# Kernel optimization log

Measured on AMD Instinct MI355X. Metric: run time of the kernel, lower is better.

## Reference

```python
import jax, jax.numpy as jnp
import numpy as np

DECAY = 0.99
BETA = 0.25
EPS_NORM = 1e-12  # matches F.normalize eps


def _l2_normalize(x):
    n = jnp.linalg.norm(x, axis=-1, keepdims=True)
    return x / jnp.maximum(n, EPS_NORM)


def setup_inputs() -> dict:
    key = jax.random.key(0)
    ks = jax.random.split(key, 8)
    B, C, H, W = 16, 256, 64, 64
    D, K = 16, 4096  # codebook_dim, n_embed
    z = jax.random.normal(ks[0], (B, C, H, W), dtype=jnp.float32)
    # 1x1 convs == per-pixel linear layers
    w_down = jax.random.normal(ks[1], (D, C), dtype=jnp.float32) / np.sqrt(C).astype(np.float32)
    b_down = jnp.zeros((D,), dtype=jnp.float32)
    w_up = jax.random.normal(ks[2], (C, D), dtype=jnp.float32) / np.sqrt(D).astype(np.float32)
    b_up = jnp.zeros((C,), dtype=jnp.float32)
    embedding = jax.random.uniform(ks[3], (K, D), minval=-1.0 / K, maxval=1.0 / K, dtype=jnp.float32)
    cluster_size = jax.random.uniform(ks[4], (K,), minval=0.5, maxval=2.0, dtype=jnp.float32)
    embed_avg = jax.random.normal(ks[5], (K, D), dtype=jnp.float32) * 0.01
    return {"z": z, "w_down": w_down, "b_down": b_down, "w_up": w_up,
            "b_up": b_up, "embedding": embedding,
            "cluster_size": cluster_size, "embed_avg": embed_avg}


def reference(z, w_down, b_down, w_up, b_up, embedding, cluster_size, embed_avg):
    B, C, H, W = z.shape
    K, D = embedding.shape

    # proj_down: 1x1 conv -> per-token linear
    z_low = jnp.einsum('bchw,dc->bdhw', z, w_down) + b_down[None, :, None, None]
    z_flat = z_low.transpose(0, 2, 3, 1).reshape(-1, D)          # [N, D]
    z_norm = _l2_normalize(z_flat)
    e_norm = _l2_normalize(embedding)                             # [K, D]

    # squared L2 distances (argmin identical to cdist argmin)
    d2 = (jnp.sum(z_norm * z_norm, -1, keepdims=True)
          - 2.0 * z_norm @ e_norm.T
          + jnp.sum(e_norm * e_norm, -1)[None, :])               # [N, K]
    indices = jnp.argmin(d2, axis=-1)                             # [N]
    z_q_flat = e_norm[indices]                                    # [N, D]

    # EMA buffer update (training path); scatter-accumulate via segment_sum
    ones = jnp.ones(indices.shape, dtype=jnp.float32)
    batch_cluster_size = jax.ops.segment_sum(ones, indices, num_segments=K)
    batch_embed_sum = jax.ops.segment_sum(z_norm, indices, num_segments=K)
    new_cluster_size = cluster_size * DECAY + (1.0 - DECAY) * batch_cluster_size
    new_embed_avg = embed_avg * DECAY + (1.0 - DECAY) * batch_embed_sum
    n = new_cluster_size.sum()
    cs = (new_cluster_size + 1e-5) / (n + K * 1e-5) * n
    new_embedding = new_embed_avg / cs[:, None]

    commitment_loss = BETA * jnp.mean((z_norm - jax.lax.stop_gradient(z_q_flat)) ** 2)

    # straight-through estimator
    z_q_low_flat = z_norm + jax.lax.stop_gradient(z_q_flat - z_norm)
    z_q_low = z_q_low_flat.reshape(B, H, W, D).transpose(0, 3, 1, 2)
    z_q = jnp.einsum('bdhw,cd->bchw', z_q_low, w_up) + b_up[None, :, None, None]

    indices_2d = indices.reshape(B, H, W)

    # metrics / entropy loss (usage == bincount(indices))
    usage_prob = batch_cluster_size / (batch_cluster_size.sum() + 1e-8)
    entropy = -jnp.sum(usage_prob * jnp.log(usage_prob + 1e-8))
    entropy_loss = jnp.log(jnp.float32(K)) - entropy

    return (z_q, commitment_loss, indices_2d, entropy_loss,
            new_embedding, new_cluster_size, new_embed_avg)
```

## Files before the change

kernel.cpp:

```cpp
#include <hip/hip_runtime.h>
#include <math.h>

#define NTOK 65536
#define CDIM 256
#define DDIM 16
#define KCOD 4096
#define HWSZ 4096

#define KSPLIT 16
#define CPS (KCOD / KSPLIT)
#define TPT 4
#define TBLK (256 * TPT)

#define WS_ENORM 0
#define WS_ENN   (WS_ENORM + KCOD*DDIM)
#define WS_WDT   (WS_ENN + KCOD)
#define WS_ZN    (WS_WDT + CDIM*DDIM)
#define WS_BCS   (WS_ZN + NTOK*DDIM)
#define WS_BES   (WS_BCS + KCOD)
#define WS_SCAL  (WS_BES + KCOD*DDIM)
#define WS_PACK  (WS_SCAL + 8)

#define OFS_ZQ   0
#define OFS_LOSS 16777216
#define OFS_IDX  16777217
#define OFS_ENT  16842753
#define OFS_NE   16842754
#define OFS_NCS  16908290
#define OFS_NEA  16912386

__global__ __launch_bounds__(256) void knorm_kernel(const float* __restrict__ emb,
                                                    const float* __restrict__ w_down,
                                                    float* __restrict__ ws) {
  int k = blockIdx.x * 256 + threadIdx.x;
  const float4* src = (const float4*)emb + (size_t)k * 4;
  float4 t0 = src[0], t1 = src[1], t2 = src[2], t3 = src[3];
  float e[16] = {t0.x,t0.y,t0.z,t0.w, t1.x,t1.y,t1.z,t1.w,
                 t2.x,t2.y,t2.z,t2.w, t3.x,t3.y,t3.z,t3.w};
  float ss = 0.f;
  #pragma unroll
  for (int d = 0; d < 16; ++d) ss += e[d] * e[d];
  float dn = fmaxf(sqrtf(ss), 1e-12f);
  #pragma unroll
  for (int d = 0; d < 16; ++d) e[d] = e[d] / dn;
  float s2 = 0.f;
  #pragma unroll
  for (int d = 0; d < 16; ++d) s2 += e[d] * e[d];
  float4* dst = (float4*)(ws + WS_ENORM) + (size_t)k * 4;
  dst[0] = make_float4(e[0],e[1],e[2],e[3]);
  dst[1] = make_float4(e[4],e[5],e[6],e[7]);
  dst[2] = make_float4(e[8],e[9],e[10],e[11]);
  dst[3] = make_float4(e[12],e[13],e[14],e[15]);
  ws[WS_ENN + k] = s2;
  ws[WS_WDT + k] = w_down[(k & 15) * 256 + (k >> 4)];
}

__global__ __launch_bounds__(256) void kdown_kernel(const float* __restrict__ z,
                                                    const float* __restrict__ wdt,
                                                    const float* __restrict__ b_down,
                                                    float* __restrict__ znp) {
  const int tid = threadIdx.x;
  const int n = blockIdx.x * 256 + tid;
  const int b = n >> 12;
  const int hw = n & 4095;

  const float* zp = z + (size_t)b * (CDIM * HWSZ) + hw;
  float acc[16];
  #pragma unroll
  for (int d = 0; d < 16; ++d) acc[d] = 0.f;
  #pragma unroll 8
  for (int c = 0; c < CDIM; ++c) {
    float zv = zp[(size_t)c * HWSZ];
    const float4* wr = (const float4*)(wdt + c * 16);
    float4 w0 = wr[0], w1 = wr[1], w2 = wr[2], w3 = wr[3];
    acc[0]  = fmaf(zv, w0.x, acc[0]);  acc[1]  = fmaf(zv, w0.y, acc[1]);
    acc[2]  = fmaf(zv, w0.z, acc[2]);  acc[3]  = fmaf(zv, w0.w, acc[3]);
    acc[4]  = fmaf(zv, w1.x, acc[4]);  acc[5]  = fmaf(zv, w1.y, acc[5]);
    acc[6]  = fmaf(zv, w1.z, acc[6]);  acc[7]  = fmaf(zv, w1.w, acc[7]);
    acc[8]  = fmaf(zv, w2.x, acc[8]);  acc[9]  = fmaf(zv, w2.y, acc[9]);
    acc[10] = fmaf(zv, w2.z, acc[10]); acc[11] = fmaf(zv, w2.w, acc[11]);
    acc[12] = fmaf(zv, w3.x, acc[12]); acc[13] = fmaf(zv, w3.y, acc[13]);
    acc[14] = fmaf(zv, w3.z, acc[14]); acc[15] = fmaf(zv, w3.w, acc[15]);
  }
  #pragma unroll
  for (int d = 0; d < 16; ++d) acc[d] = acc[d] + b_down[d];
  float ss = 0.f;
  #pragma unroll
  for (int d = 0; d < 16; ++d) ss += acc[d] * acc[d];
  float dn = fmaxf(sqrtf(ss), 1e-12f);
  float zn[16];
  #pragma unroll
  for (int d = 0; d < 16; ++d) zn[d] = acc[d] / dn;

  float4* op = (float4*)znp + (size_t)n * 4;
  op[0] = make_float4(zn[0],zn[1],zn[2],zn[3]);
  op[1] = make_float4(zn[4],zn[5],zn[6],zn[7]);
  op[2] = make_float4(zn[8],zn[9],zn[10],zn[11]);
  op[3] = make_float4(zn[12],zn[13],zn[14],zn[15]);
}

__global__ __launch_bounds__(256, 4) void kscan_kernel(const float* __restrict__ enorm,
                                                       const float* __restrict__ ennp,
                                                       const float* __restrict__ znp,
                                                       unsigned long long* __restrict__ packp) {
  __shared__ float ecache[CPS * DDIM];
  __shared__ float encache[CPS];

  const int tid = threadIdx.x;
  const int kbase = blockIdx.y * CPS;

  {
    const float4* s4 = (const float4*)(enorm + (size_t)kbase * 16);
    float4* d4 = (float4*)ecache;
    #pragma unroll
    for (int i = 0; i < 4; ++i) d4[tid + i * 256] = s4[tid + i * 256];
    encache[tid] = ennp[kbase + tid];
  }
  __syncthreads();

  float nz[TPT][16];
  float best[TPT];
  int bidx[TPT];
  const int tokbase = blockIdx.x * TBLK + tid;
  {
    const float4* zp = (const float4*)znp;
    #pragma unroll
    for (int p = 0; p < TPT; ++p) {
      int tok = tokbase + p * 256;
      float4 a0 = zp[(size_t)tok * 4 + 0];
      float4 a1 = zp[(size_t)tok * 4 + 1];
      float4 a2 = zp[(size_t)tok * 4 + 2];
      float4 a3 = zp[(size_t)tok * 4 + 3];
      nz[p][0]=-2.f*a0.x; nz[p][1]=-2.f*a0.y; nz[p][2]=-2.f*a0.z; nz[p][3]=-2.f*a0.w;
      nz[p][4]=-2.f*a1.x; nz[p][5]=-2.f*a1.y; nz[p][6]=-2.f*a1.z; nz[p][7]=-2.f*a1.w;
      nz[p][8]=-2.f*a2.x; nz[p][9]=-2.f*a2.y; nz[p][10]=-2.f*a2.z; nz[p][11]=-2.f*a2.w;
      nz[p][12]=-2.f*a3.x; nz[p][13]=-2.f*a3.y; nz[p][14]=-2.f*a3.z; nz[p][15]=-2.f*a3.w;
      best[p] = 3.4e38f;
      bidx[p] = 0;
    }
  }

  #pragma unroll 2
  for (int j = 0; j < CPS; ++j) {
    const float4* e4 = (const float4*)(ecache + j * 16);
    float4 c0 = e4[0], c1 = e4[1], c2 = e4[2], c3 = e4[3];
    float en = encache[j];
    #pragma unroll
    for (int p = 0; p < TPT; ++p) {
      float d = en;
      d = fmaf(nz[p][0],  c0.x, d); d = fmaf(nz[p][1],  c0.y, d);
      d = fmaf(nz[p][2],  c0.z, d); d = fmaf(nz[p][3],  c0.w, d);
      d = fmaf(nz[p][4],  c1.x, d); d = fmaf(nz[p][5],  c1.y, d);
      d = fmaf(nz[p][6],  c1.z, d); d = fmaf(nz[p][7],  c1.w, d);
      d = fmaf(nz[p][8],  c2.x, d); d = fmaf(nz[p][9],  c2.y, d);
      d = fmaf(nz[p][10], c2.z, d); d = fmaf(nz[p][11], c2.w, d);
      d = fmaf(nz[p][12], c3.x, d); d = fmaf(nz[p][13], c3.y, d);
      d = fmaf(nz[p][14], c3.z, d); d = fmaf(nz[p][15], c3.w, d);
      if (d < best[p]) { best[p] = d; bidx[p] = j; }
    }
  }

  #pragma unroll
  for (int p = 0; p < TPT; ++p) {
    int tok = tokbase + p * 256;
    unsigned u = __float_as_uint(best[p]);
    u = (u & 0x80000000u) ? ~u : (u | 0x80000000u);
    unsigned long long key =
        ((unsigned long long)u << 32) | (unsigned)(kbase + bidx[p]);
    atomicMin(packp + tok, key);
  }
}

__global__ __launch_bounds__(256) void kfinal_kernel(const float* __restrict__ w_up,
                                                     const float* __restrict__ b_up,
                                                     const float* __restrict__ enorm,
                                                     const float* __restrict__ znp,
                                                     const unsigned long long* __restrict__ packp,
                                                     float* __restrict__ wsacc,
                                                     float* __restrict__ out) {
  const int tid = threadIdx.x;
  const int n = blockIdx.x * 256 + tid;
  const int bidx = (int)(unsigned)(packp[n] & 0xFFFFFFFFull);

  float zn[16];
  {
    const float4* zp = (const float4*)znp + (size_t)n * 4;
    float4 a0 = zp[0], a1 = zp[1], a2 = zp[2], a3 = zp[3];
    zn[0]=a0.x; zn[1]=a0.y; zn[2]=a0.z; zn[3]=a0.w;
    zn[4]=a1.x; zn[5]=a1.y; zn[6]=a1.z; zn[7]=a1.w;
    zn[8]=a2.x; zn[9]=a2.y; zn[10]=a2.z; zn[11]=a2.w;
    zn[12]=a3.x; zn[13]=a3.y; zn[14]=a3.z; zn[15]=a3.w;
  }
  float zq[16];
  {
    const float4* eb = (const float4*)enorm + (size_t)bidx * 4;
    float4 q0 = eb[0], q1 = eb[1], q2 = eb[2], q3 = eb[3];
    zq[0]=q0.x; zq[1]=q0.y; zq[2]=q0.z; zq[3]=q0.w;
    zq[4]=q1.x; zq[5]=q1.y; zq[6]=q1.z; zq[7]=q1.w;
    zq[8]=q2.x; zq[9]=q2.y; zq[10]=q2.z; zq[11]=q2.w;
    zq[12]=q3.x; zq[13]=q3.y; zq[14]=q3.z; zq[15]=q3.w;
  }

  out[OFS_IDX + n] = (float)bidx;

  float ls = 0.f;
  #pragma unroll
  for (int d = 0; d < 16; ++d) { float df = zn[d] - zq[d]; ls = fmaf(df, df, ls); }

  atomicAdd(wsacc + WS_BCS - WS_BCS + bidx, 1.0f);
  #pragma unroll
  for (int d = 0; d < 16; ++d)
    atomicAdd(wsacc + KCOD + (size_t)bidx * 16 + d, zn[d]);

  #pragma unroll
  for (int off = 32; off > 0; off >>= 1) ls += __shfl_down(ls, off, 64);
  if ((tid & 63) == 0) atomicAdd(wsacc + KCOD + KCOD * DDIM + 0, ls);

  float ql[16];
  #pragma unroll
  for (int d = 0; d < 16; ++d) ql[d] = zn[d] + (zq[d] - zn[d]);

  const int b = n >> 12, hw = n & 4095;
  float* op = out + OFS_ZQ + (size_t)b * (CDIM * HWSZ) + hw;
  #pragma unroll 8
  for (int c = 0; c < CDIM; ++c) {
    const float4* wr = (const float4*)(w_up + c * 16);
    float4 w0 = wr[0], w1 = wr[1], w2 = wr[2], w3 = wr[3];
    float a = 0.f;
    a = fmaf(ql[0],  w0.x, a); a = fmaf(ql[1],  w0.y, a);
    a = fmaf(ql[2],  w0.z, a); a = fmaf(ql[3],  w0.w, a);
    a = fmaf(ql[4],  w1.x, a); a = fmaf(ql[5],  w1.y, a);
    a = fmaf(ql[6],  w1.z, a); a = fmaf(ql[7],  w1.w, a);
    a = fmaf(ql[8],  w2.x, a); a = fmaf(ql[9],  w2.y, a);
    a = fmaf(ql[10], w2.z, a); a = fmaf(ql[11], w2.w, a);
    a = fmaf(ql[12], w3.x, a); a = fmaf(ql[13], w3.y, a);
    a = fmaf(ql[14], w3.z, a); a = fmaf(ql[15], w3.w, a);
    a = a + b_up[c];
    op[(size_t)c * HWSZ] = a;
  }
}

__global__ __launch_bounds__(256) void kema_kernel(const float* __restrict__ cluster_size,
                                                   const float* __restrict__ embed_avg,
                                                   float* __restrict__ ws,
                                                   float* __restrict__ out) {
  const float DEC = 0.99f;
  const float OMD = (float)(1.0 - 0.99);
  const int k = blockIdx.x * 256 + threadIdx.x;
  float bcsv = ws[WS_BCS + k];
  float ncs = cluster_size[k] * DEC + OMD * bcsv;
  out[OFS_NCS + k] = ncs;
  #pragma unroll
  for (int d = 0; d < 16; ++d) {
    float nea = embed_avg[(size_t)k * 16 + d] * DEC + OMD * ws[WS_BES + (size_t)k * 16 + d];
    out[OFS_NEA + (size_t)k * 16 + d] = nea;
  }
  float p = bcsv / 65536.0f;
  float et = -p * logf(p + 1e-8f);

  __shared__ float r1[4], r2[4];
  float v1 = ncs, v2 = et;
  #pragma unroll
  for (int off = 32; off > 0; off >>= 1) {
    v1 += __shfl_down(v1, off, 64);
    v2 += __shfl_down(v2, off, 64);
  }
  int lane = threadIdx.x & 63, w = threadIdx.x >> 6;
  if (lane == 0) { r1[w] = v1; r2[w] = v2; }
  __syncthreads();
  if (threadIdx.x == 0) {
    atomicAdd(ws + WS_SCAL + 1, (r1[0] + r1[1]) + (r1[2] + r1[3]));
    atomicAdd(ws + WS_SCAL + 2, (r2[0] + r2[1]) + (r2[2] + r2[3]));
  }
}

__global__ __launch_bounds__(256) void kemb_kernel(const float* __restrict__ ws,
                                                   float* __restrict__ out) {
  const float KEPS = (float)(4096.0 * 1e-5);
  const int k = blockIdx.x * 256 + threadIdx.x;
  float n = ws[WS_SCAL + 1];
  float ncs = out[OFS_NCS + k];
  float cs = (ncs + 1e-5f) / (n + KEPS) * n;
  #pragma unroll
  for (int d = 0; d < 16; ++d)
    out[OFS_NE + (size_t)k * 16 + d] = out[OFS_NEA + (size_t)k * 16 + d] / cs;
  if (k == 0) {
    out[OFS_LOSS] = 0.25f * (ws[WS_SCAL + 0] / 1048576.0f);
    out[OFS_ENT]  = (float)8.317766166719343 - ws[WS_SCAL + 2];
  }
}

extern "C" void kernel_launch(void* const* d_in, const int* in_sizes, int n_in,
                              void* d_out, int out_size, void* d_ws, size_t ws_size,
                              hipStream_t stream) {
  const float* z        = (const float*)d_in[0];
  const float* w_down   = (const float*)d_in[1];
  const float* b_down   = (const float*)d_in[2];
  const float* w_up     = (const float*)d_in[3];
  const float* b_up     = (const float*)d_in[4];
  const float* emb      = (const float*)d_in[5];
  const float* csz      = (const float*)d_in[6];
  const float* eavg     = (const float*)d_in[7];
  float* out = (float*)d_out;
  float* ws  = (float*)d_ws;

  hipMemsetAsync(ws + WS_BCS, 0, (size_t)(KCOD + KCOD*DDIM + 8) * sizeof(float), stream);
  hipMemsetAsync(ws + WS_PACK, 0xFF, (size_t)NTOK * 8, stream);

  knorm_kernel<<<KCOD / 256, 256, 0, stream>>>(emb, w_down, ws);
  kdown_kernel<<<NTOK / 256, 256, 0, stream>>>(z, ws + WS_WDT, b_down, ws + WS_ZN);
  kscan_kernel<<<dim3(NTOK / TBLK, KSPLIT), 256, 0, stream>>>(
      ws + WS_ENORM, ws + WS_ENN, ws + WS_ZN,
      (unsigned long long*)(ws + WS_PACK));
  kfinal_kernel<<<NTOK / 256, 256, 0, stream>>>(
      w_up, b_up, ws + WS_ENORM, ws + WS_ZN,
      (const unsigned long long*)(ws + WS_PACK), ws + WS_BCS, out);
  kema_kernel<<<KCOD / 256, 256, 0, stream>>>(csz, eavg, ws, out);
  kemb_kernel<<<KCOD / 256, 256, 0, stream>>>(ws, out);
}
```

Baseline: 271.6 us.

## Stage projection weights in LDS, process two tokens per thread, widen scan tile

```diff
diff --git a/kernel.cpp b/kernel.cpp
--- a/kernel.cpp
+++ b/kernel.cpp
@@ -9,7 +9,7 @@
 
 #define KSPLIT 16
 #define CPS (KCOD / KSPLIT)
-#define TPT 4
+#define TPT 8
 #define TBLK (256 * TPT)
 
 #define WS_ENORM 0
@@ -55,51 +55,85 @@
   ws[WS_WDT + k] = w_down[(k & 15) * 256 + (k >> 4)];
 }
 
-__global__ __launch_bounds__(256) void kdown_kernel(const float* __restrict__ z,
-                                                    const float* __restrict__ wdt,
-                                                    const float* __restrict__ b_down,
-                                                    float* __restrict__ znp) {
+__global__ __launch_bounds__(128, 2) void kdown_kernel(const float* __restrict__ z,
+                                                       const float* __restrict__ wdt,
+                                                       const float* __restrict__ b_down,
+                                                       float* __restrict__ znp) {
+  __shared__ float wdT[CDIM * DDIM];
   const int tid = threadIdx.x;
-  const int n = blockIdx.x * 256 + tid;
-  const int b = n >> 12;
-  const int hw = n & 4095;
-
+  {
+    const float4* s4 = (const float4*)wdt;
+    float4* d4 = (float4*)wdT;
+    #pragma unroll
+    for (int i = 0; i < 8; ++i) d4[tid + i * 128] = s4[tid + i * 128];
+  }
+  float bd[16];
+  {
+    const float4* bp = (const float4*)b_down;
+    float4 b0 = bp[0], b1 = bp[1], b2 = bp[2], b3 = bp[3];
+    bd[0]=b0.x; bd[1]=b0.y; bd[2]=b0.z; bd[3]=b0.w;
+    bd[4]=b1.x; bd[5]=b1.y; bd[6]=b1.z; bd[7]=b1.w;
+    bd[8]=b2.x; bd[9]=b2.y; bd[10]=b2.z; bd[11]=b2.w;
+    bd[12]=b3.x; bd[13]=b3.y; bd[14]=b3.z; bd[15]=b3.w;
+  }
+  __syncthreads();
+
+  const int n0 = blockIdx.x * 256 + tid;
+  const int b = n0 >> 12;
+  const int hw = n0 & 4095;
   const float* zp = z + (size_t)b * (CDIM * HWSZ) + hw;
-  float acc[16];
-  #pragma unroll
-  for (int d = 0; d < 16; ++d) acc[d] = 0.f;
-  #pragma unroll 8
+
+  float a0[16], a1[16];
+  #pragma unroll
+  for (int d = 0; d < 16; ++d) { a0[d] = 0.f; a1[d] = 0.f; }
+
+  #pragma unroll 16
   for (int c = 0; c < CDIM; ++c) {
-    float zv = zp[(size_t)c * HWSZ];
-    const float4* wr = (const float4*)(wdt + c * 16);
+    float zv0 = zp[(size_t)c * HWSZ];
+    float zv1 = zp[(size_t)c * HWSZ + 128];
+    const float4* wr = (const float4*)(wdT + c * 16);
     float4 w0 = wr[0], w1 = wr[1], w2 = wr[2], w3 = wr[3];
-    acc[0]  = fmaf(zv, w0.x, acc[0]);  acc[1]  = fmaf(zv, w0.y, acc[1]);
-    acc[2]  = fmaf(zv, w0.z, acc[2]);  acc[3]  = fmaf(zv, w0.w, acc[3]);
-    acc[4]  = fmaf(zv, w1.x, acc[4]);  acc[5]  = fmaf(zv, w1.y, acc[5]);
-    acc[6]  = fmaf(zv, w1.z, acc[6]);  acc[7]  = fmaf(zv, w1.w, acc[7]);
-    acc[8]  = fmaf(zv, w2.x, acc[8]);  acc[9]  = fmaf(zv, w2.y, acc[9]);
-    acc[10] = fmaf(zv, w2.z, acc[10]); acc[11] = fmaf(zv, w2.w, acc[11]);
-    acc[12] = fmaf(zv, w3.x, acc[12]); acc[13] = fmaf(zv, w3.y, acc[13]);
-    acc[14] = fmaf(zv, w3.z, acc[14]); acc[15] = fmaf(zv, w3.w, acc[15]);
-  }
-  #pragma unroll
-  for (int d = 0; d < 16; ++d) acc[d] = acc[d] + b_down[d];
-  float ss = 0.f;
-  #pragma unroll
-  for (int d = 0; d < 16; ++d) ss += acc[d] * acc[d];
-  float dn = fmaxf(sqrtf(ss), 1e-12f);
-  float zn[16];
-  #pragma unroll
-  for (int d = 0; d < 16; ++d) zn[d] = acc[d] / dn;
-
-  float4* op = (float4*)znp + (size_t)n * 4;
-  op[0] = make_float4(zn[0],zn[1],zn[2],zn[3]);
-  op[1] = make_float4(zn[4],zn[5],zn[6],zn[7]);
-  op[2] = make_float4(zn[8],zn[9],zn[10],zn[11]);
-  op[3] = make_float4(zn[12],zn[13],zn[14],zn[15]);
-}
-
-__global__ __launch_bounds__(256, 4) void kscan_kernel(const float* __restrict__ enorm,
+    a0[0]  = fmaf(zv0, w0.x, a0[0]);  a1[0]  = fmaf(zv1, w0.x, a1[0]);
+    a0[1]  = fmaf(zv0, w0.y, a0[1]);  a1[1]  = fmaf(zv1, w0.y, a1[1]);
+    a0[2]  = fmaf(zv0, w0.z, a0[2]);  a1[2]  = fmaf(zv1, w0.z, a1[2]);
+    a0[3]  = fmaf(zv0, w0.w, a0[3]);  a1[3]  = fmaf(zv1, w0.w, a1[3]);
+    a0[4]  = fmaf(zv0, w1.x, a0[4]);  a1[4]  = fmaf(zv1, w1.x, a1[4]);
+    a0[5]  = fmaf(zv0, w1.y, a0[5]);  a1[5]  = fmaf(zv1, w1.y, a1[5]);
+    a0[6]  = fmaf(zv0, w1.z, a0[6]);  a1[6]  = fmaf(zv1, w1.z, a1[6]);
+    a0[7]  = fmaf(zv0, w1.w, a0[7]);  a1[7]  = fmaf(zv1, w1.w, a1[7]);
+    a0[8]  = fmaf(zv0, w2.x, a0[8]);  a1[8]  = fmaf(zv1, w2.x, a1[8]);
+    a0[9]  = fmaf(zv0, w2.y, a0[9]);  a1[9]  = fmaf(zv1, w2.y, a1[9]);
+    a0[10] = fmaf(zv0, w2.z, a0[10]); a1[10] = fmaf(zv1, w2.z, a1[10]);
+    a0[11] = fmaf(zv0, w2.w, a0[11]); a1[11] = fmaf(zv1, w2.w, a1[11]);
+    a0[12] = fmaf(zv0, w3.x, a0[12]); a1[12] = fmaf(zv1, w3.x, a1[12]);
+    a0[13] = fmaf(zv0, w3.y, a0[13]); a1[13] = fmaf(zv1, w3.y, a1[13]);
+    a0[14] = fmaf(zv0, w3.z, a0[14]); a1[14] = fmaf(zv1, w3.z, a1[14]);
+    a0[15] = fmaf(zv0, w3.w, a0[15]); a1[15] = fmaf(zv1, w3.w, a1[15]);
+  }
+
+  #pragma unroll
+  for (int d = 0; d < 16; ++d) { a0[d] += bd[d]; a1[d] += bd[d]; }
+  float s0 = 0.f, s1 = 0.f;
+  #pragma unroll
+  for (int d = 0; d < 16; ++d) { s0 += a0[d] * a0[d]; s1 += a1[d] * a1[d]; }
+  float dn0 = fmaxf(sqrtf(s0), 1e-12f);
+  float dn1 = fmaxf(sqrtf(s1), 1e-12f);
+  #pragma unroll
+  for (int d = 0; d < 16; ++d) { a0[d] /= dn0; a1[d] /= dn1; }
+
+  float4* op0 = (float4*)znp + (size_t)n0 * 4;
+  float4* op1 = (float4*)znp + (size_t)(n0 + 128) * 4;
+  op0[0] = make_float4(a0[0],a0[1],a0[2],a0[3]);
+  op0[1] = make_float4(a0[4],a0[5],a0[6],a0[7]);
+  op0[2] = make_float4(a0[8],a0[9],a0[10],a0[11]);
+  op0[3] = make_float4(a0[12],a0[13],a0[14],a0[15]);
+  op1[0] = make_float4(a1[0],a1[1],a1[2],a1[3]);
+  op1[1] = make_float4(a1[4],a1[5],a1[6],a1[7]);
+  op1[2] = make_float4(a1[8],a1[9],a1[10],a1[11]);
+  op1[3] = make_float4(a1[12],a1[13],a1[14],a1[15]);
+}
+
+__global__ __launch_bounds__(256, 2) void kscan_kernel(const float* __restrict__ enorm,
                                                        const float* __restrict__ ennp,
                                                        const float* __restrict__ znp,
                                                        unsigned long long* __restrict__ packp) {
@@ -171,72 +205,92 @@
   }
 }
 
-__global__ __launch_bounds__(256) void kfinal_kernel(const float* __restrict__ w_up,
-                                                     const float* __restrict__ b_up,
-                                                     const float* __restrict__ enorm,
-                                                     const float* __restrict__ znp,
-                                                     const unsigned long long* __restrict__ packp,
-                                                     float* __restrict__ wsacc,
-                                                     float* __restrict__ out) {
+__global__ __launch_bounds__(128, 2) void kfinal_kernel(const float* __restrict__ w_up,
+                                                        const float* __restrict__ b_up,
+                                                        const float* __restrict__ enorm,
+                                                        const float* __restrict__ znp,
+                                                        const unsigned long long* __restrict__ packp,
+                                                        float* __restrict__ wsacc,
+                                                        float* __restrict__ out) {
+  __shared__ float wu[CDIM * DDIM];
+  __shared__ float bu[CDIM];
   const int tid = threadIdx.x;
-  const int n = blockIdx.x * 256 + tid;
-  const int bidx = (int)(unsigned)(packp[n] & 0xFFFFFFFFull);
-
-  float zn[16];
-  {
-    const float4* zp = (const float4*)znp + (size_t)n * 4;
-    float4 a0 = zp[0], a1 = zp[1], a2 = zp[2], a3 = zp[3];
-    zn[0]=a0.x; zn[1]=a0.y; zn[2]=a0.z; zn[3]=a0.w;
-    zn[4]=a1.x; zn[5]=a1.y; zn[6]=a1.z; zn[7]=a1.w;
-    zn[8]=a2.x; zn[9]=a2.y; zn[10]=a2.z; zn[11]=a2.w;
-    zn[12]=a3.x; zn[13]=a3.y; zn[14]=a3.z; zn[15]=a3.w;
-  }
-  float zq[16];
-  {
-    const float4* eb = (const float4*)enorm + (size_t)bidx * 4;
-    float4 q0 = eb[0], q1 = eb[1], q2 = eb[2], q3 = eb[3];
-    zq[0]=q0.x; zq[1]=q0.y; zq[2]=q0.z; zq[3]=q0.w;
-    zq[4]=q1.x; zq[5]=q1.y; zq[6]=q1.z; zq[7]=q1.w;
-    zq[8]=q2.x; zq[9]=q2.y; zq[10]=q2.z; zq[11]=q2.w;
-    zq[12]=q3.x; zq[13]=q3.y; zq[14]=q3.z; zq[15]=q3.w;
-  }
-
-  out[OFS_IDX + n] = (float)bidx;
-
+  {
+    const float4* s4 = (const float4*)w_up;
+    float4* d4 = (float4*)wu;
+    #pragma unroll
+    for (int i = 0; i < 8; ++i) d4[tid + i * 128] = s4[tid + i * 128];
+    bu[tid] = b_up[tid];
+    bu[tid + 128] = b_up[tid + 128];
+  }
+  __syncthreads();
+
+  const int n0 = blockIdx.x * 256 + tid;
   float ls = 0.f;
-  #pragma unroll
-  for (int d = 0; d < 16; ++d) { float df = zn[d] - zq[d]; ls = fmaf(df, df, ls); }
-
-  atomicAdd(wsacc + WS_BCS - WS_BCS + bidx, 1.0f);
-  #pragma unroll
-  for (int d = 0; d < 16; ++d)
-    atomicAdd(wsacc + KCOD + (size_t)bidx * 16 + d, zn[d]);
+  float ql0[16], ql1[16];
+
+  #pragma unroll
+  for (int t = 0; t < 2; ++t) {
+    const int n = n0 + t * 128;
+    const int bidx = (int)(unsigned)(packp[n] & 0xFFFFFFFFull);
+    float zn[16], zq[16];
+    {
+      const float4* zp = (const float4*)znp + (size_t)n * 4;
+      float4 a0 = zp[0], a1 = zp[1], a2 = zp[2], a3 = zp[3];
+      zn[0]=a0.x; zn[1]=a0.y; zn[2]=a0.z; zn[3]=a0.w;
+      zn[4]=a1.x; zn[5]=a1.y; zn[6]=a1.z; zn[7]=a1.w;
+      zn[8]=a2.x; zn[9]=a2.y; zn[10]=a2.z; zn[11]=a2.w;
+      zn[12]=a3.x; zn[13]=a3.y; zn[14]=a3.z; zn[15]=a3.w;
+    }
+    {
+      const float4* eb = (const float4*)enorm + (size_t)bidx * 4;
+      float4 q0 = eb[0], q1 = eb[1], q2 = eb[2], q3 = eb[3];
+      zq[0]=q0.x; zq[1]=q0.y; zq[2]=q0.z; zq[3]=q0.w;
+      zq[4]=q1.x; zq[5]=q1.y; zq[6]=q1.z; zq[7]=q1.w;
+      zq[8]=q2.x; zq[9]=q2.y; zq[10]=q2.z; zq[11]=q2.w;
+      zq[12]=q3.x; zq[13]=q3.y; zq[14]=q3.z; zq[15]=q3.w;
+    }
+    out[OFS_IDX + n] = (float)bidx;
+    #pragma unroll
+    for (int d = 0; d < 16; ++d) { float df = zn[d] - zq[d]; ls = fmaf(df, df, ls); }
+    atomicAdd(wsacc + bidx, 1.0f);
+    #pragma unroll
+    for (int d = 0; d < 16; ++d)
+      atomicAdd(wsacc + KCOD + (size_t)bidx * 16 + d, zn[d]);
+    float* ql = t ? ql1 : ql0;
+    #pragma unroll
+    for (int d = 0; d < 16; ++d) ql[d] = zn[d] + (zq[d] - zn[d]);
+  }
 
   #pragma unroll
   for (int off = 32; off > 0; off >>= 1) ls += __shfl_down(ls, off, 64);
   if ((tid & 63) == 0) atomicAdd(wsacc + KCOD + KCOD * DDIM + 0, ls);
 
-  float ql[16];
-  #pragma unroll
-  for (int d = 0; d < 16; ++d) ql[d] = zn[d] + (zq[d] - zn[d]);
-
-  const int b = n >> 12, hw = n & 4095;
+  const int b = n0 >> 12, hw = n0 & 4095;
   float* op = out + OFS_ZQ + (size_t)b * (CDIM * HWSZ) + hw;
   #pragma unroll 8
   for (int c = 0; c < CDIM; ++c) {
-    const float4* wr = (const float4*)(w_up + c * 16);
+    const float4* wr = (const float4*)(wu + c * 16);
     float4 w0 = wr[0], w1 = wr[1], w2 = wr[2], w3 = wr[3];
-    float a = 0.f;
-    a = fmaf(ql[0],  w0.x, a); a = fmaf(ql[1],  w0.y, a);
-    a = fmaf(ql[2],  w0.z, a); a = fmaf(ql[3],  w0.w, a);
-    a = fmaf(ql[4],  w1.x, a); a = fmaf(ql[5],  w1.y, a);
-    a = fmaf(ql[6],  w1.z, a); a = fmaf(ql[7],  w1.w, a);
-    a = fmaf(ql[8],  w2.x, a); a = fmaf(ql[9],  w2.y, a);
-    a = fmaf(ql[10], w2.z, a); a = fmaf(ql[11], w2.w, a);
-    a = fmaf(ql[12], w3.x, a); a = fmaf(ql[13], w3.y, a);
-    a = fmaf(ql[14], w3.z, a); a = fmaf(ql[15], w3.w, a);
-    a = a + b_up[c];
-    op[(size_t)c * HWSZ] = a;
+    float a = 0.f, a2 = 0.f;
+    a  = fmaf(ql0[0],  w0.x, a);  a2 = fmaf(ql1[0],  w0.x, a2);
+    a  = fmaf(ql0[1],  w0.y, a);  a2 = fmaf(ql1[1],  w0.y, a2);
+    a  = fmaf(ql0[2],  w0.z, a);  a2 = fmaf(ql1[2],  w0.z, a2);
+    a  = fmaf(ql0[3],  w0.w, a);  a2 = fmaf(ql1[3],  w0.w, a2);
+    a  = fmaf(ql0[4],  w1.x, a);  a2 = fmaf(ql1[4],  w1.x, a2);
+    a  = fmaf(ql0[5],  w1.y, a);  a2 = fmaf(ql1[5],  w1.y, a2);
+    a  = fmaf(ql0[6],  w1.z, a);  a2 = fmaf(ql1[6],  w1.z, a2);
+    a  = fmaf(ql0[7],  w1.w, a);  a2 = fmaf(ql1[7],  w1.w, a2);
+    a  = fmaf(ql0[8],  w2.x, a);  a2 = fmaf(ql1[8],  w2.x, a2);
+    a  = fmaf(ql0[9],  w2.y, a);  a2 = fmaf(ql1[9],  w2.y, a2);
+    a  = fmaf(ql0[10], w2.z, a);  a2 = fmaf(ql1[10], w2.z, a2);
+    a  = fmaf(ql0[11], w2.w, a);  a2 = fmaf(ql1[11], w2.w, a2);
+    a  = fmaf(ql0[12], w3.x, a);  a2 = fmaf(ql1[12], w3.x, a2);
+    a  = fmaf(ql0[13], w3.y, a);  a2 = fmaf(ql1[13], w3.y, a2);
+    a  = fmaf(ql0[14], w3.z, a);  a2 = fmaf(ql1[14], w3.z, a2);
+    a  = fmaf(ql0[15], w3.w, a);  a2 = fmaf(ql1[15], w3.w, a2);
+    op[(size_t)c * HWSZ] = a + bu[c];
+    op[(size_t)c * HWSZ + 128] = a2 + bu[c];
   }
 }
 
@@ -308,11 +362,11 @@
   hipMemsetAsync(ws + WS_PACK, 0xFF, (size_t)NTOK * 8, stream);
 
   knorm_kernel<<<KCOD / 256, 256, 0, stream>>>(emb, w_down, ws);
-  kdown_kernel<<<NTOK / 256, 256, 0, stream>>>(z, ws + WS_WDT, b_down, ws + WS_ZN);
+  kdown_kernel<<<NTOK / 256, 128, 0, stream>>>(z, ws + WS_WDT, b_down, ws + WS_ZN);
   kscan_kernel<<<dim3(NTOK / TBLK, KSPLIT), 256, 0, stream>>>(
       ws + WS_ENORM, ws + WS_ENN, ws + WS_ZN,
       (unsigned long long*)(ws + WS_PACK));
-  kfinal_kernel<<<NTOK / 256, 256, 0, stream>>>(
+  kfinal_kernel<<<NTOK / 256, 128, 0, stream>>>(
       w_up, b_up, ws + WS_ENORM, ws + WS_ZN,
       (const unsigned long long*)(ws + WS_PACK), ws + WS_BCS, out);
   kema_kernel<<<KCOD / 256, 256, 0, stream>>>(csz, eavg, ws, out);
```

New measurement: 254.6 us. -6.3%, faster.

## Fuse codebook normalization into scan/final kernels and stage weights in LDS

Applied to the files above, without the earlier changes.

```diff
diff --git a/kernel.cpp b/kernel.cpp
--- a/kernel.cpp
+++ b/kernel.cpp
@@ -9,13 +9,10 @@
 
 #define KSPLIT 16
 #define CPS (KCOD / KSPLIT)
-#define TPT 4
+#define TPT 8
 #define TBLK (256 * TPT)
 
-#define WS_ENORM 0
-#define WS_ENN   (WS_ENORM + KCOD*DDIM)
-#define WS_WDT   (WS_ENN + KCOD)
-#define WS_ZN    (WS_WDT + CDIM*DDIM)
+#define WS_ZN    0
 #define WS_BCS   (WS_ZN + NTOK*DDIM)
 #define WS_BES   (WS_BCS + KCOD)
 #define WS_SCAL  (WS_BES + KCOD*DDIM)
@@ -29,49 +26,31 @@
 #define OFS_NCS  16908290
 #define OFS_NEA  16912386
 
-__global__ __launch_bounds__(256) void knorm_kernel(const float* __restrict__ emb,
-                                                    const float* __restrict__ w_down,
-                                                    float* __restrict__ ws) {
-  int k = blockIdx.x * 256 + threadIdx.x;
-  const float4* src = (const float4*)emb + (size_t)k * 4;
-  float4 t0 = src[0], t1 = src[1], t2 = src[2], t3 = src[3];
-  float e[16] = {t0.x,t0.y,t0.z,t0.w, t1.x,t1.y,t1.z,t1.w,
-                 t2.x,t2.y,t2.z,t2.w, t3.x,t3.y,t3.z,t3.w};
-  float ss = 0.f;
-  #pragma unroll
-  for (int d = 0; d < 16; ++d) ss += e[d] * e[d];
-  float dn = fmaxf(sqrtf(ss), 1e-12f);
-  #pragma unroll
-  for (int d = 0; d < 16; ++d) e[d] = e[d] / dn;
-  float s2 = 0.f;
-  #pragma unroll
-  for (int d = 0; d < 16; ++d) s2 += e[d] * e[d];
-  float4* dst = (float4*)(ws + WS_ENORM) + (size_t)k * 4;
-  dst[0] = make_float4(e[0],e[1],e[2],e[3]);
-  dst[1] = make_float4(e[4],e[5],e[6],e[7]);
-  dst[2] = make_float4(e[8],e[9],e[10],e[11]);
-  dst[3] = make_float4(e[12],e[13],e[14],e[15]);
-  ws[WS_ENN + k] = s2;
-  ws[WS_WDT + k] = w_down[(k & 15) * 256 + (k >> 4)];
-}
-
-__global__ __launch_bounds__(256) void kdown_kernel(const float* __restrict__ z,
-                                                    const float* __restrict__ wdt,
-                                                    const float* __restrict__ b_down,
-                                                    float* __restrict__ znp) {
+__global__ __attribute__((amdgpu_flat_work_group_size(256, 256), amdgpu_waves_per_eu(1, 4)))
+void kdown_kernel(const float* __restrict__ z,
+                  const float* __restrict__ w_down,
+                  const float* __restrict__ b_down,
+                  float* __restrict__ znp) {
+  __shared__ float wdT[CDIM * DDIM];
   const int tid = threadIdx.x;
+  for (int i = tid; i < CDIM * DDIM; i += 256) {
+    wdT[(i & 255) * 16 + (i >> 8)] = w_down[i];
+  }
+  __syncthreads();
+
   const int n = blockIdx.x * 256 + tid;
   const int b = n >> 12;
   const int hw = n & 4095;
-
   const float* zp = z + (size_t)b * (CDIM * HWSZ) + hw;
+
   float acc[16];
   #pragma unroll
   for (int d = 0; d < 16; ++d) acc[d] = 0.f;
-  #pragma unroll 8
+
+  #pragma unroll 32
   for (int c = 0; c < CDIM; ++c) {
     float zv = zp[(size_t)c * HWSZ];
-    const float4* wr = (const float4*)(wdt + c * 16);
+    const float4* wr = (const float4*)(wdT + c * 16);
     float4 w0 = wr[0], w1 = wr[1], w2 = wr[2], w3 = wr[3];
     acc[0]  = fmaf(zv, w0.x, acc[0]);  acc[1]  = fmaf(zv, w0.y, acc[1]);
     acc[2]  = fmaf(zv, w0.z, acc[2]);  acc[3]  = fmaf(zv, w0.w, acc[3]);
@@ -82,27 +61,27 @@
     acc[12] = fmaf(zv, w3.x, acc[12]); acc[13] = fmaf(zv, w3.y, acc[13]);
     acc[14] = fmaf(zv, w3.z, acc[14]); acc[15] = fmaf(zv, w3.w, acc[15]);
   }
+
   #pragma unroll
   for (int d = 0; d < 16; ++d) acc[d] = acc[d] + b_down[d];
   float ss = 0.f;
   #pragma unroll
   for (int d = 0; d < 16; ++d) ss += acc[d] * acc[d];
   float dn = fmaxf(sqrtf(ss), 1e-12f);
-  float zn[16];
-  #pragma unroll
-  for (int d = 0; d < 16; ++d) zn[d] = acc[d] / dn;
+  #pragma unroll
+  for (int d = 0; d < 16; ++d) acc[d] = acc[d] / dn;
 
   float4* op = (float4*)znp + (size_t)n * 4;
-  op[0] = make_float4(zn[0],zn[1],zn[2],zn[3]);
-  op[1] = make_float4(zn[4],zn[5],zn[6],zn[7]);
-  op[2] = make_float4(zn[8],zn[9],zn[10],zn[11]);
-  op[3] = make_float4(zn[12],zn[13],zn[14],zn[15]);
-}
-
-__global__ __launch_bounds__(256, 4) void kscan_kernel(const float* __restrict__ enorm,
-                                                       const float* __restrict__ ennp,
-                                                       const float* __restrict__ znp,
-                                                       unsigned long long* __restrict__ packp) {
+  op[0] = make_float4(acc[0],acc[1],acc[2],acc[3]);
+  op[1] = make_float4(acc[4],acc[5],acc[6],acc[7]);
+  op[2] = make_float4(acc[8],acc[9],acc[10],acc[11]);
+  op[3] = make_float4(acc[12],acc[13],acc[14],acc[15]);
+}
+
+__global__ __attribute__((amdgpu_flat_work_group_size(256, 256), amdgpu_waves_per_eu(2, 2)))
+void kscan_kernel(const float* __restrict__ emb,
+                  const float* __restrict__ znp,
+                  unsigned long long* __restrict__ packp) {
   __shared__ float ecache[CPS * DDIM];
   __shared__ float encache[CPS];
 
@@ -110,11 +89,25 @@
   const int kbase = blockIdx.y * CPS;
 
   {
-    const float4* s4 = (const float4*)(enorm + (size_t)kbase * 16);
-    float4* d4 = (float4*)ecache;
-    #pragma unroll
-    for (int i = 0; i < 4; ++i) d4[tid + i * 256] = s4[tid + i * 256];
-    encache[tid] = ennp[kbase + tid];
+    const float4* er = (const float4*)(emb + (size_t)(kbase + tid) * 16);
+    float4 t0 = er[0], t1 = er[1], t2 = er[2], t3 = er[3];
+    float e[16] = {t0.x,t0.y,t0.z,t0.w, t1.x,t1.y,t1.z,t1.w,
+                   t2.x,t2.y,t2.z,t2.w, t3.x,t3.y,t3.z,t3.w};
+    float ss = 0.f;
+    #pragma unroll
+    for (int d = 0; d < 16; ++d) ss += e[d] * e[d];
+    float dn = fmaxf(sqrtf(ss), 1e-12f);
+    #pragma unroll
+    for (int d = 0; d < 16; ++d) e[d] = e[d] / dn;
+    float s2 = 0.f;
+    #pragma unroll
+    for (int d = 0; d < 16; ++d) s2 += e[d] * e[d];
+    float4* ec = (float4*)(ecache + tid * 16);
+    ec[0] = make_float4(e[0],e[1],e[2],e[3]);
+    ec[1] = make_float4(e[4],e[5],e[6],e[7]);
+    ec[2] = make_float4(e[8],e[9],e[10],e[11]);
+    ec[3] = make_float4(e[12],e[13],e[14],e[15]);
+    encache[tid] = s2;
   }
   __syncthreads();
 
@@ -171,14 +164,26 @@
   }
 }
 
-__global__ __launch_bounds__(256) void kfinal_kernel(const float* __restrict__ w_up,
-                                                     const float* __restrict__ b_up,
-                                                     const float* __restrict__ enorm,
-                                                     const float* __restrict__ znp,
-                                                     const unsigned long long* __restrict__ packp,
-                                                     float* __restrict__ wsacc,
-                                                     float* __restrict__ out) {
+__global__ __attribute__((amdgpu_flat_work_group_size(256, 256), amdgpu_waves_per_eu(1, 4)))
+void kfinal_kernel(const float* __restrict__ w_up,
+                   const float* __restrict__ b_up,
+                   const float* __restrict__ emb,
+                   const float* __restrict__ znp,
+                   const unsigned long long* __restrict__ packp,
+                   float* __restrict__ wsacc,
+                   float* __restrict__ out) {
+  __shared__ float wu[CDIM * DDIM];
+  __shared__ float bu[CDIM];
   const int tid = threadIdx.x;
+  {
+    const float4* s4 = (const float4*)w_up;
+    float4* d4 = (float4*)wu;
+    #pragma unroll
+    for (int i = 0; i < 4; ++i) d4[tid + i * 256] = s4[tid + i * 256];
+    bu[tid] = b_up[tid];
+  }
+  __syncthreads();
+
   const int n = blockIdx.x * 256 + tid;
   const int bidx = (int)(unsigned)(packp[n] & 0xFFFFFFFFull);
 
@@ -193,12 +198,18 @@
   }
   float zq[16];
   {
-    const float4* eb = (const float4*)enorm + (size_t)bidx * 4;
+    const float4* eb = (const float4*)(emb + (size_t)bidx * 16);
     float4 q0 = eb[0], q1 = eb[1], q2 = eb[2], q3 = eb[3];
     zq[0]=q0.x; zq[1]=q0.y; zq[2]=q0.z; zq[3]=q0.w;
     zq[4]=q1.x; zq[5]=q1.y; zq[6]=q1.z; zq[7]=q1.w;
     zq[8]=q2.x; zq[9]=q2.y; zq[10]=q2.z; zq[11]=q2.w;
     zq[12]=q3.x; zq[13]=q3.y; zq[14]=q3.z; zq[15]=q3.w;
+    float ss = 0.f;
+    #pragma unroll
+    for (int d = 0; d < 16; ++d) ss += zq[d] * zq[d];
+    float dn = fmaxf(sqrtf(ss), 1e-12f);
+    #pragma unroll
+    for (int d = 0; d < 16; ++d) zq[d] = zq[d] / dn;
   }
 
   out[OFS_IDX + n] = (float)bidx;
@@ -207,7 +218,7 @@
   #pragma unroll
   for (int d = 0; d < 16; ++d) { float df = zn[d] - zq[d]; ls = fmaf(df, df, ls); }
 
-  atomicAdd(wsacc + WS_BCS - WS_BCS + bidx, 1.0f);
+  atomicAdd(wsacc + bidx, 1.0f);
   #pragma unroll
   for (int d = 0; d < 16; ++d)
     atomicAdd(wsacc + KCOD + (size_t)bidx * 16 + d, zn[d]);
@@ -222,9 +233,9 @@
 
   const int b = n >> 12, hw = n & 4095;
   float* op = out + OFS_ZQ + (size_t)b * (CDIM * HWSZ) + hw;
-  #pragma unroll 8
+  #pragma unroll 16
   for (int c = 0; c < CDIM; ++c) {
-    const float4* wr = (const float4*)(w_up + c * 16);
+    const float4* wr = (const float4*)(wu + c * 16);
     float4 w0 = wr[0], w1 = wr[1], w2 = wr[2], w3 = wr[3];
     float a = 0.f;
     a = fmaf(ql[0],  w0.x, a); a = fmaf(ql[1],  w0.y, a);
@@ -235,7 +246,7 @@
     a = fmaf(ql[10], w2.z, a); a = fmaf(ql[11], w2.w, a);
     a = fmaf(ql[12], w3.x, a); a = fmaf(ql[13], w3.y, a);
     a = fmaf(ql[14], w3.z, a); a = fmaf(ql[15], w3.w, a);
-    a = a + b_up[c];
+    a = a + bu[c];
     op[(size_t)c * HWSZ] = a;
   }
 }
@@ -307,13 +318,11 @@
   hipMemsetAsync(ws + WS_BCS, 0, (size_t)(KCOD + KCOD*DDIM + 8) * sizeof(float), stream);
   hipMemsetAsync(ws + WS_PACK, 0xFF, (size_t)NTOK * 8, stream);
 
-  knorm_kernel<<<KCOD / 256, 256, 0, stream>>>(emb, w_down, ws);
-  kdown_kernel<<<NTOK / 256, 256, 0, stream>>>(z, ws + WS_WDT, b_down, ws + WS_ZN);
+  kdown_kernel<<<NTOK / 256, 256, 0, stream>>>(z, w_down, b_down, ws + WS_ZN);
   kscan_kernel<<<dim3(NTOK / TBLK, KSPLIT), 256, 0, stream>>>(
-      ws + WS_ENORM, ws + WS_ENN, ws + WS_ZN,
-      (unsigned long long*)(ws + WS_PACK));
+      emb, ws + WS_ZN, (unsigned long long*)(ws + WS_PACK));
   kfinal_kernel<<<NTOK / 256, 256, 0, stream>>>(
-      w_up, b_up, ws + WS_ENORM, ws + WS_ZN,
+      w_up, b_up, emb, ws + WS_ZN,
       (const unsigned long long*)(ws + WS_PACK), ws + WS_BCS, out);
   kema_kernel<<<KCOD / 256, 256, 0, stream>>>(csz, eavg, ws, out);
   kemb_kernel<<<KCOD / 256, 256, 0, stream>>>(ws, out);
```

Measured after the change: 262.9 us. 3.2% less time.
